# Performance work log

Measured on AMD Instinct MI355X. Metric: run time of the kernel, lower is better.

The kernel has to match this reference:

```python
import jax, jax.numpy as jnp
import numpy as np

N_NODES = 100000


def gcn_conv(x, W, b, src, dst, n):
    # PyG GCNConv: xW, add self-loops, symmetric normalization, scatter-add, +bias
    xw = x @ W                                   # [N, out]
    loop = jnp.arange(n, dtype=src.dtype)
    s = jnp.concatenate([src, loop])             # [E+N]
    d = jnp.concatenate([dst, loop])             # [E+N]
    deg = jax.ops.segment_sum(jnp.ones_like(d, dtype=xw.dtype), d, num_segments=n)
    dis = jnp.where(deg > 0, jax.lax.rsqrt(jnp.maximum(deg, 1e-12)), 0.0)
    norm = dis[s] * dis[d]                       # [E+N]
    msg = xw[s] * norm[:, None]                  # [E+N, out]  (gather + scale)
    out = jax.ops.segment_sum(msg, d, num_segments=n)  # scatter-add
    return out + b


def setup_inputs() -> dict:
    key = jax.random.key(0)
    k1, k2, k3, k4 = jax.random.split(key, 4)
    x = jax.random.normal(k1, (N_NODES, 128), dtype=jnp.float32)
    edge_index = jax.random.randint(k2, (2, 1600000), 0, N_NODES, dtype=jnp.int64)
    W1 = jax.random.normal(k3, (128, 64), dtype=jnp.float32) * (1.0 / np.sqrt(128))
    b1 = jnp.zeros((64,), dtype=jnp.float32)
    W2 = jax.random.normal(k4, (64, 40), dtype=jnp.float32) * (1.0 / np.sqrt(64))
    b2 = jnp.zeros((40,), dtype=jnp.float32)
    return {"x": x, "edge_index": edge_index, "W1": W1, "b1": b1, "W2": W2, "b2": b2}


def reference(x, edge_index, W1, b1, W2, b2):
    src, dst = edge_index[0], edge_index[1]
    n = x.shape[0]
    h = gcn_conv(x, W1, b1, src, dst, n)
    h = jax.nn.relu(h)
    # dropout p=0.6 is identity in eval mode (training=False)
    h = gcn_conv(h, W2, b2, src, dst, n)
    return jax.nn.log_softmax(h, axis=1)
```

## Files before the change

### kernel.cpp

```cpp
#include <hip/hip_runtime.h>
#include <math.h>

typedef unsigned short u16;
typedef unsigned int u32;
typedef __attribute__((ext_vector_type(2))) float f32x2;
typedef __attribute__((ext_vector_type(4))) float f32x4;
typedef __attribute__((ext_vector_type(8))) short short8;

#define CAP 64
#define BSHIFT 9
#define BCAP 9600

__device__ inline float bf2f(u16 u) {
    union { u32 i; float f; } c; c.i = ((u32)u) << 16; return c.f;
}
__device__ inline u16 f2bf(float f) {
    union { float f; u32 i; } c; c.f = f;
    u32 r = c.i + 0x7FFFu + ((c.i >> 16) & 1u);
    return (u16)(r >> 16);
}
__device__ inline u32 cvtpk(float lo, float hi) {
    u32 r;
    asm("v_cvt_pk_bf16_f32 %0, %1, %2" : "=v"(r) : "v"(lo), "v"(hi));
    return r;
}
__device__ inline f32x2 unp(u32 d) {
    union { u32 u; float f; } lo, hi;
    lo.u = d << 16;
    hi.u = d & 0xFFFF0000u;
    f32x2 r; r.x = lo.f; r.y = hi.f;
    return r;
}
__device__ inline f32x2 shflx2(f32x2 val, int m) {
    union { f32x2 v; int u[2]; } a; a.v = val;
    a.u[0] = __shfl_xor(a.u[0], m);
    a.u[1] = __shfl_xor(a.u[1], m);
    return a.v;
}


__global__ void zero_gcount_kernel(int* __restrict__ gcount) {
    gcount[threadIdx.x] = 0;
}

__global__ __launch_bounds__(256) void bucket_kernel(const int* __restrict__ src,
                                                     const int* __restrict__ dst,
                                                     int* __restrict__ gcount,
                                                     int2* __restrict__ bucketbuf,
                                                     int e, int nb) {
    __shared__ int lh[256];
    int tid = threadIdx.x;
    if (tid < nb) lh[tid] = 0;
    __syncthreads();
    int per = (e + gridDim.x - 1) / gridDim.x;
    int i0 = blockIdx.x * per;
    int i1 = i0 + per; if (i1 > e) i1 = e;
    for (int i = i0 + tid; i < i1; i += 256)
        atomicAdd(&lh[dst[i] >> BSHIFT], 1);
    __syncthreads();
    if (tid < nb) {
        int c = lh[tid];
        lh[tid] = (c > 0) ? atomicAdd(&gcount[tid], c) : 0;
    }
    __syncthreads();
    for (int i = i0 + tid; i < i1; i += 256) {
        int d = dst[i], s = src[i];
        int b = d >> BSHIFT;
        int pos = atomicAdd(&lh[b], 1);
        if (pos < BCAP) bucketbuf[(size_t)b * BCAP + pos] = make_int2(d, s);
    }
}

__global__ __launch_bounds__(256) void csrify_kernel(const int2* __restrict__ bucketbuf,
                                                     const int* __restrict__ gcount,
                                                     int* __restrict__ cnt,
                                                     float* __restrict__ dis,
                                                     int* __restrict__ srcs2d, int n) {
    __shared__ int lc[512];
    int b = blockIdx.x;
    int tid = threadIdx.x;
    int node_lo = b << BSHIFT;
    #pragma unroll
    for (int q = tid; q < 512; q += 256) lc[q] = 0;
    __syncthreads();
    int m = gcount[b]; if (m > BCAP) m = BCAP;
    const int2* bp = bucketbuf + (size_t)b * BCAP;
    for (int i = tid; i < m; i += 256) {
        int2 r = bp[i];
        int k = atomicAdd(&lc[r.x - node_lo], 1);
        if (k < CAP - 1) srcs2d[((size_t)r.x << 6) + k + 1] = r.y;
    }
    __syncthreads();
    for (int q = tid; q < 512; q += 256) {
        int node = node_lo + q;
        if (node < n) {
            int c = lc[q];
            int nr = (c < CAP - 1 ? c : CAP - 1) + 1;
            cnt[node] = nr;
            dis[node] = rsqrtf((float)c + 1.0f);
            int* row = srcs2d + ((size_t)node << 6);
            row[0] = node;
            int pr = (nr + 7) & ~7;
            for (int t = nr; t < pr; ++t) row[t] = n;
        }
    }
}


template<typename XT, int IN_F, int OUT_F>
__global__ __launch_bounds__(256) void gemm_mfma_kernel(const XT* __restrict__ X,
                                                        const float* __restrict__ W,
                                                        const float* __restrict__ dis,
                                                        u16* __restrict__ Y, int n) {
    constexpr int KP = IN_F + 8;
    constexpr int NKS = IN_F / 32;
    __shared__ u16 Wt[64 * KP];
    int tid = threadIdx.x;
    for (int idx = tid; idx < 64 * IN_F; idx += 256) {
        int c = idx / IN_F, k = idx % IN_F;
        float v = (c < OUT_F) ? W[k * OUT_F + c] : 0.f;
        Wt[c * KP + k] = f2bf(v);
    }
    __syncthreads();
    int l = tid & 63;
    int w = tid >> 6;
    int lm = l & 15;
    int g4 = (l >> 4) << 2;

    short8 Wf[4][NKS];
    #pragma unroll
    for (int ct = 0; ct < 4; ++ct) {
        const u16* wp = &Wt[(ct * 16 + lm) * KP + g4];
        #pragma unroll
        for (int ks = 0; ks < NKS; ++ks) {
            union { short8 s; uint2 u[2]; } b;
            b.u[0] = *(const uint2*)(wp + ks * 32);
            b.u[1] = *(const uint2*)(wp + ks * 32 + 16);
            Wf[ct][ks] = b.s;
        }
    }

    #pragma unroll
    for (int rt = 0; rt < 2; ++rt) {
        int rw = blockIdx.x * 128 + rt * 64 + w * 16;
        int ra = rw + lm;
        if (ra >= n) ra = n - 1;
        short8 Xf[NKS];
        if (sizeof(XT) == 4) {
            const float* xp = (const float*)X + (size_t)ra * IN_F + g4;
            #pragma unroll
            for (int ks = 0; ks < NKS; ++ks) {
                float4 f1 = *(const float4*)(xp + ks * 32);
                float4 f2 = *(const float4*)(xp + ks * 32 + 16);
                union { short8 s; u32 d[4]; } a;
                a.d[0] = cvtpk(f1.x, f1.y);
                a.d[1] = cvtpk(f1.z, f1.w);
                a.d[2] = cvtpk(f2.x, f2.y);
                a.d[3] = cvtpk(f2.z, f2.w);
                Xf[ks] = a.s;
            }
        } else {
            const u16* xp = (const u16*)X + (size_t)ra * IN_F + g4;
            #pragma unroll
            for (int ks = 0; ks < NKS; ++ks) {
                union { short8 s; uint2 u[2]; } a;
                a.u[0] = *(const uint2*)(xp + ks * 32);
                a.u[1] = *(const uint2*)(xp + ks * 32 + 16);
                Xf[ks] = a.s;
            }
        }
        f32x4 acc[4] = {};
        #pragma unroll
        for (int ks = 0; ks < NKS; ++ks)
            #pragma unroll
            for (int ct = 0; ct < 4; ++ct)
                acc[ct] = __builtin_amdgcn_mfma_f32_16x16x32_bf16(Wf[ct][ks], Xf[ks], acc[ct], 0, 0, 0);
        int r = rw + lm;
        if (r < n) {
            float sc = dis[r];
            #pragma unroll
            for (int ct = 0; ct < 4; ++ct) {
                uint2 p;
                p.x = cvtpk(acc[ct][0] * sc, acc[ct][1] * sc);
                p.y = cvtpk(acc[ct][2] * sc, acc[ct][3] * sc);
                *(uint2*)(Y + (size_t)r * 64 + ct * 16 + g4) = p;
            }
        } else if (r == n) {
            #pragma unroll
            for (int ct = 0; ct < 4; ++ct)
                *(uint2*)(Y + (size_t)n * 64 + ct * 16 + g4) = make_uint2(0u, 0u);
        }
    }
}


template<int FINAL>
__global__ __launch_bounds__(64) void gatherw_kernel(const u16* __restrict__ v,
                                                     const int* __restrict__ cnt,
                                                     const int* __restrict__ srcs2d,
                                                     const float* __restrict__ dis,
                                                     const float* __restrict__ bias,
                                                     u16* __restrict__ outb,
                                                     float* __restrict__ outf, int n) {
    int wid0 = blockIdx.x * 2;
    int wid1 = wid0 + 1;
    int lane = threadIdx.x;
    int j = lane >> 3;
    int c = lane & 7;
    u32 coff = (u32)(c << 3);

    int nr0 = __builtin_amdgcn_readfirstlane(cnt[wid0]);
    int p0 = (nr0 + 7) & ~7;
    bool has1 = wid1 < n;
    int nr1 = has1 ? __builtin_amdgcn_readfirstlane(cnt[wid1]) : 0;
    int p1 = has1 ? ((nr1 + 7) & ~7) : 0;
    int pm = p0 > p1 ? p0 : p1;

    int idx0 = srcs2d[((size_t)wid0 << 6) + lane];
    int idx1 = srcs2d[((size_t)(has1 ? wid1 : wid0) << 6) + lane];

    f32x2 acc0[4], acc1[4];
    #pragma unroll
    for (int i = 0; i < 4; ++i) {
        acc0[i].x = 0.f; acc0[i].y = 0.f;
        acc1[i].x = 0.f; acc1[i].y = 0.f;
    }
    int baddr = j << 2;
    for (int k = 0; k < pm; k += 8) {
        int sj0 = __builtin_amdgcn_ds_bpermute(baddr, idx0);
        int sj1 = __builtin_amdgcn_ds_bpermute(baddr, idx1);
        baddr += 32;
        if (k >= p0) sj0 = n;
        if (k >= p1) sj1 = n;
        uint4 a0 = *(const uint4*)(v + (((u32)sj0 << 6) + coff));
        uint4 a1 = *(const uint4*)(v + (((u32)sj1 << 6) + coff));
        acc0[0] += unp(a0.x); acc0[1] += unp(a0.y);
        acc0[2] += unp(a0.z); acc0[3] += unp(a0.w);
        acc1[0] += unp(a1.x); acc1[1] += unp(a1.y);
        acc1[2] += unp(a1.z); acc1[3] += unp(a1.w);
    }
    #pragma unroll
    for (int i = 0; i < 4; ++i) {
        acc0[i] += shflx2(acc0[i], 8);
        acc0[i] += shflx2(acc0[i], 16);
        acc0[i] += shflx2(acc0[i], 32);
        acc1[i] += shflx2(acc1[i], 8);
        acc1[i] += shflx2(acc1[i], 16);
        acc1[i] += shflx2(acc1[i], 32);
    }

    #pragma unroll
    for (int g = 0; g < 2; ++g) {
        int wid = g == 0 ? wid0 : wid1;
        if (g == 1 && !has1) break;
        f32x2* acc = g == 0 ? acc0 : acc1;
        float di = dis[wid];
        if (FINAL == 0) {
            const f32x2* bp2 = (const f32x2*)(bias + (c << 3));
            f32x2 o[4];
            #pragma unroll
            for (int i = 0; i < 4; ++i) {
                f32x2 b = bp2[i];
                o[i].x = fmaxf(fmaf(di, acc[i].x, b.x), 0.f);
                o[i].y = fmaxf(fmaf(di, acc[i].y, b.y), 0.f);
            }
            if (j == 0) {
                uint4 p = make_uint4(cvtpk(o[0].x, o[0].y), cvtpk(o[1].x, o[1].y),
                                     cvtpk(o[2].x, o[2].y), cvtpk(o[3].x, o[3].y));
                *(uint4*)(outb + (((size_t)wid) << 6) + (c << 3)) = p;
            }
        } else {
            bool act = c < 5;
            int cb = act ? c : 0;
            const f32x2* bp2 = (const f32x2*)(bias + (cb << 3));
            float zz[8];
            #pragma unroll
            for (int i = 0; i < 4; ++i) {
                f32x2 b = bp2[i];
                zz[2 * i]     = act ? fmaf(di, acc[i].x, b.x) : -INFINITY;
                zz[2 * i + 1] = act ? fmaf(di, acc[i].y, b.y) : -INFINITY;
            }
            float mx = zz[0];
            #pragma unroll
            for (int i = 1; i < 8; ++i) mx = fmaxf(mx, zz[i]);
            mx = fmaxf(mx, __shfl_xor(mx, 1));
            mx = fmaxf(mx, __shfl_xor(mx, 2));
            mx = fmaxf(mx, __shfl_xor(mx, 4));
            float ssum = 0.f;
            if (act) {
                #pragma unroll
                for (int i = 0; i < 8; ++i) ssum += __expf(zz[i] - mx);
            }
            ssum += __shfl_xor(ssum, 1);
            ssum += __shfl_xor(ssum, 2);
            ssum += __shfl_xor(ssum, 4);
            float ls = __logf(ssum) + mx;
            if (j == 0 && act) {
                float* op = outf + (size_t)wid * 40 + (c << 3);
                *(float4*)op = make_float4(zz[0] - ls, zz[1] - ls, zz[2] - ls, zz[3] - ls);
                *(float4*)(op + 4) = make_float4(zz[4] - ls, zz[5] - ls, zz[6] - ls, zz[7] - ls);
            }
        }
    }
}


extern "C" void kernel_launch(void* const* d_in, const int* in_sizes, int n_in,
                              void* d_out, int out_size, void* d_ws, size_t ws_size,
                              hipStream_t stream) {
    const float* x  = (const float*)d_in[0];
    const int*   ei = (const int*)d_in[1];
    const float* W1 = (const float*)d_in[2];
    const float* b1 = (const float*)d_in[3];
    const float* W2 = (const float*)d_in[4];
    const float* b2 = (const float*)d_in[5];
    float* out = (float*)d_out;

    const int n = in_sizes[0] / 128;
    const int e = in_sizes[1] / 2;
    const int* src = ei;
    const int* dst = ei + e;
    const int nb = (n + 511) >> BSHIFT;

    int* gcount = (int*)d_ws;
    int* cnt    = gcount + 256;
    float* dis  = (float*)(cnt + n);
    int2* bucketbuf = (int2*)(dis + n);
    u16* A      = (u16*)bucketbuf;
    int* srcs2d = (int*)(bucketbuf + (size_t)nb * BCAP);
    u16* B      = (u16*)(srcs2d + ((size_t)n << 6));

    const int mblocks = (n + 128) / 128;
    const int gwblocks = (n + 1) / 2;

    zero_gcount_kernel<<<1, 256, 0, stream>>>(gcount);
    bucket_kernel<<<448, 256, 0, stream>>>(src, dst, gcount, bucketbuf, e, nb);
    csrify_kernel<<<nb, 256, 0, stream>>>(bucketbuf, gcount, cnt, dis, srcs2d, n);

    gemm_mfma_kernel<float, 128, 64>
        <<<mblocks, 256, 0, stream>>>(x, W1, dis, A, n);
    gatherw_kernel<0><<<gwblocks, 64, 0, stream>>>(A, cnt, srcs2d, dis, b1, B, nullptr, n);

    gemm_mfma_kernel<u16, 64, 40>
        <<<mblocks, 256, 0, stream>>>(B, W2, dis, A, n);
    gatherw_kernel<1><<<gwblocks, 64, 0, stream>>>(A, cnt, srcs2d, dis, b2, nullptr, out, n);
}
```

Baseline: 255.5 us.

## Reorder second GCN layer to aggregate first, then apply W2 inside gather

Removes the second GEMM kernel by using associativity: layer-1 output is pre-scaled by dis and stored as bf16 with 64 features, layer 2 gathers these 64-wide rows and then multiplies by W2 (staged in LDS) inside the gather kernel before log_softmax. This drops one kernel launch and one full write and read of the intermediate matrix. In exchange, the second gather moves 64 features per edge instead of 40, and it adds per-node matvec work and an LDS staging step in every block.

```diff
diff --git a/kernel.cpp b/kernel.cpp
--- a/kernel.cpp
+++ b/kernel.cpp
@@ -200,14 +200,23 @@
                                                      const int* __restrict__ srcs2d,
                                                      const float* __restrict__ dis,
                                                      const float* __restrict__ bias,
+                                                     const float* __restrict__ W2mat,
                                                      u16* __restrict__ outb,
                                                      float* __restrict__ outf, int n) {
+    __shared__ float W2l[FINAL ? 2560 : 1];
     int wid0 = blockIdx.x * 2;
     int wid1 = wid0 + 1;
     int lane = threadIdx.x;
     int j = lane >> 3;
     int c = lane & 7;
     u32 coff = (u32)(c << 3);
+
+    if (FINAL == 1) {
+        const float4* g4p = (const float4*)(W2mat + lane * 40);
+        float4* s4p = (float4*)(W2l + lane * 40);
+        #pragma unroll
+        for (int i = 0; i < 10; ++i) s4p[i] = g4p[i];
+    }
 
     int nr0 = __builtin_amdgcn_readfirstlane(cnt[wid0]);
     int p0 = (nr0 + 7) & ~7;
@@ -249,56 +258,80 @@
         acc1[i] += shflx2(acc1[i], 32);
     }
 
-    #pragma unroll
-    for (int g = 0; g < 2; ++g) {
-        int wid = g == 0 ? wid0 : wid1;
-        if (g == 1 && !has1) break;
-        f32x2* acc = g == 0 ? acc0 : acc1;
-        float di = dis[wid];
-        if (FINAL == 0) {
+    if (FINAL == 0) {
+        #pragma unroll
+        for (int g = 0; g < 2; ++g) {
+            int wid = g == 0 ? wid0 : wid1;
+            if (g == 1 && !has1) break;
+            f32x2* acc = g == 0 ? acc0 : acc1;
+            float di = dis[wid];
             const f32x2* bp2 = (const f32x2*)(bias + (c << 3));
             f32x2 o[4];
             #pragma unroll
             for (int i = 0; i < 4; ++i) {
                 f32x2 b = bp2[i];
-                o[i].x = fmaxf(fmaf(di, acc[i].x, b.x), 0.f);
-                o[i].y = fmaxf(fmaf(di, acc[i].y, b.y), 0.f);
+                o[i].x = fmaxf(fmaf(di, acc[i].x, b.x), 0.f) * di;
+                o[i].y = fmaxf(fmaf(di, acc[i].y, b.y), 0.f) * di;
             }
             if (j == 0) {
                 uint4 p = make_uint4(cvtpk(o[0].x, o[0].y), cvtpk(o[1].x, o[1].y),
                                      cvtpk(o[2].x, o[2].y), cvtpk(o[3].x, o[3].y));
                 *(uint4*)(outb + (((size_t)wid) << 6) + (c << 3)) = p;
             }
-        } else {
-            bool act = c < 5;
-            int cb = act ? c : 0;
-            const f32x2* bp2 = (const f32x2*)(bias + (cb << 3));
-            float zz[8];
+        }
+        if (wid0 == 0 && j == 0)
+            *(uint4*)(outb + (((size_t)n) << 6) + (c << 3)) = make_uint4(0u, 0u, 0u, 0u);
+    } else {
+        __syncthreads();
+        float w2f[8][5];
+        #pragma unroll
+        for (int f8 = 0; f8 < 8; ++f8)
+            #pragma unroll
+            for (int q = 0; q < 5; ++q)
+                w2f[f8][q] = W2l[((c << 3) + f8) * 40 + j * 5 + q];
+        float bq[5];
+        #pragma unroll
+        for (int q = 0; q < 5; ++q) bq[q] = bias[j * 5 + q];
+
+        #pragma unroll
+        for (int g = 0; g < 2; ++g) {
+            int wid = g == 0 ? wid0 : wid1;
+            if (g == 1 && !has1) break;
+            f32x2* acc = g == 0 ? acc0 : acc1;
+            float zp[5] = {0.f, 0.f, 0.f, 0.f, 0.f};
             #pragma unroll
             for (int i = 0; i < 4; ++i) {
-                f32x2 b = bp2[i];
-                zz[2 * i]     = act ? fmaf(di, acc[i].x, b.x) : -INFINITY;
-                zz[2 * i + 1] = act ? fmaf(di, acc[i].y, b.y) : -INFINITY;
-            }
-            float mx = zz[0];
-            #pragma unroll
-            for (int i = 1; i < 8; ++i) mx = fmaxf(mx, zz[i]);
-            mx = fmaxf(mx, __shfl_xor(mx, 1));
-            mx = fmaxf(mx, __shfl_xor(mx, 2));
-            mx = fmaxf(mx, __shfl_xor(mx, 4));
+                #pragma unroll
+                for (int q = 0; q < 5; ++q) {
+                    zp[q] = fmaf(acc[i].x, w2f[2 * i][q], zp[q]);
+                    zp[q] = fmaf(acc[i].y, w2f[2 * i + 1][q], zp[q]);
+                }
+            }
+            #pragma unroll
+            for (int m = 1; m <= 4; m <<= 1)
+                #pragma unroll
+                for (int q = 0; q < 5; ++q) zp[q] += __shfl_xor(zp[q], m);
+            float di = dis[wid];
+            float Z[5];
+            #pragma unroll
+            for (int q = 0; q < 5; ++q) Z[q] = fmaf(di, zp[q], bq[q]);
+            float mx = Z[0];
+            #pragma unroll
+            for (int q = 1; q < 5; ++q) mx = fmaxf(mx, Z[q]);
+            mx = fmaxf(mx, __shfl_xor(mx, 8));
+            mx = fmaxf(mx, __shfl_xor(mx, 16));
+            mx = fmaxf(mx, __shfl_xor(mx, 32));
             float ssum = 0.f;
-            if (act) {
+            #pragma unroll
+            for (int q = 0; q < 5; ++q) ssum += __expf(Z[q] - mx);
+            ssum += __shfl_xor(ssum, 8);
+            ssum += __shfl_xor(ssum, 16);
+            ssum += __shfl_xor(ssum, 32);
+            float ls = __logf(ssum) + mx;
+            if (c == 0) {
+                float* op = outf + (size_t)wid * 40 + j * 5;
                 #pragma unroll
-                for (int i = 0; i < 8; ++i) ssum += __expf(zz[i] - mx);
-            }
-            ssum += __shfl_xor(ssum, 1);
-            ssum += __shfl_xor(ssum, 2);
-            ssum += __shfl_xor(ssum, 4);
-            float ls = __logf(ssum) + mx;
-            if (j == 0 && act) {
-                float* op = outf + (size_t)wid * 40 + (c << 3);
-                *(float4*)op = make_float4(zz[0] - ls, zz[1] - ls, zz[2] - ls, zz[3] - ls);
-                *(float4*)(op + 4) = make_float4(zz[4] - ls, zz[5] - ls, zz[6] - ls, zz[7] - ls);
+                for (int q = 0; q < 5; ++q) op[q] = Z[q] - ls;
             }
         }
     }
@@ -339,9 +372,7 @@
 
     gemm_mfma_kernel<float, 128, 64>
         <<<mblocks, 256, 0, stream>>>(x, W1, dis, A, n);
-    gatherw_kernel<0><<<gwblocks, 64, 0, stream>>>(A, cnt, srcs2d, dis, b1, B, nullptr, n);
-
-    gemm_mfma_kernel<u16, 64, 40>
-        <<<mblocks, 256, 0, stream>>>(B, W2, dis, A, n);
-    gatherw_kernel<1><<<gwblocks, 64, 0, stream>>>(A, cnt, srcs2d, dis, b2, nullptr, out, n);
-}
+    gatherw_kernel<0><<<gwblocks, 64, 0, stream>>>(A, cnt, srcs2d, dis, b1, nullptr, B, nullptr, n);
+
+    gatherw_kernel<1><<<gwblocks, 64, 0, stream>>>(B, cnt, srcs2d, dis, b2, W2, nullptr, out, n);
+}
```

After: 316.8 us. +24.0%, slower.
